# Kernel tuning notes

Measured on AMD Instinct MI355X. Metric: run time of the kernel, lower is better.

## Reference

```python
import jax, jax.numpy as jnp
import numpy as np

N = 50000
E = 800000
C = 128   # embed_channels
H = 4     # num_heads
D = C // H
POS = 3


def setup_inputs() -> dict:
    key = jax.random.key(0)
    ks = jax.random.split(key, 8)
    feat = jax.random.normal(ks[0], (N, C), dtype=jnp.float32)
    coord = jax.random.normal(ks[1], (N, POS), dtype=jnp.float32)
    graph = jax.random.randint(ks[2], (2, E), 0, N, dtype=jnp.int32)
    qkv_w = jax.random.normal(ks[3], (3 * C, C), dtype=jnp.float32) * (1.0 / np.sqrt(C))
    qkv_b = jax.random.normal(ks[4], (3 * C,), dtype=jnp.float32) * 0.02
    rpe_w = jax.random.normal(ks[5], (C, POS), dtype=jnp.float32) * (1.0 / np.sqrt(POS))
    rpe_b = jax.random.normal(ks[6], (C,), dtype=jnp.float32) * 0.02
    return {"feat": feat, "coord": coord, "graph": graph,
            "qkv_w": qkv_w, "qkv_b": qkv_b, "rpe_w": rpe_w, "rpe_b": rpe_b}


def _segment_softmax(x, seg, n):
    # x: [E, H], seg: [E] -> softmax over edges sharing the same destination node
    seg_max = jax.ops.segment_max(x, seg, num_segments=n)          # [N, H]
    seg_max = jnp.where(jnp.isfinite(seg_max), seg_max, 0.0)
    ex = jnp.exp(x - seg_max[seg])                                 # [E, H]
    seg_sum = jax.ops.segment_sum(ex, seg, num_segments=n)         # [N, H]
    return ex / seg_sum[seg]


def reference(feat, coord, graph, qkv_w, qkv_b, rpe_w, rpe_b):
    n = feat.shape[0]
    # qkv projection: [N, 3C] -> [N, 3, H, D]
    qkv = (feat @ qkv_w.T + qkv_b).reshape(n, 3, H, D)
    query, key, value = qkv[:, 0], qkv[:, 1], qkv[:, 2]            # each [N, H, D]
    dst, src = graph[0], graph[1]                                  # [E]
    # relative position encoding per edge
    rel = coord[dst] - coord[src]                                  # [E, 3]
    rpe = (rel @ rpe_w.T + rpe_b).reshape(-1, H, D)                # [E, H, D]
    # per-edge attention logits
    attn = (key[src] * query[dst] + rpe).sum(-1)                   # [E, H]
    attn = _segment_softmax(attn, dst, n)                          # [E, H]
    # weighted scatter-sum of values
    msg = attn[..., None] * value[src]                             # [E, H, D]
    out = jax.ops.segment_sum(msg, dst, num_segments=n)            # [N, H, D]
    return out.reshape(n, H * D)
```

## Files before the change

kernel.cpp:

```cpp
#include <hip/hip_runtime.h>
#include <hip/hip_bf16.h>

#define NN 50000
#define NE 800000
#define PAD 64
#define CAB 196
#define NBK 391
#define CAPB 2560
#define GB_STRIDE 32

typedef _Float16 fp16x8 __attribute__((ext_vector_type(8)));
typedef _Float16 half2 __attribute__((ext_vector_type(2)));
typedef __attribute__((ext_vector_type(8))) unsigned short ushort8;
typedef __attribute__((ext_vector_type(4))) float f32x4;

static __device__ __forceinline__ unsigned short f2h(float x) {
    _Float16 h = (_Float16)x;
    return __builtin_bit_cast(unsigned short, h);
}
static __device__ __forceinline__ float dot2(half2 a, half2 b, float c) {
#if __has_builtin(__builtin_amdgcn_fdot2)
    return __builtin_amdgcn_fdot2(a, b, c, false);
#else
    return c + (float)a.x * (float)b.x + (float)a.y * (float)b.y;
#endif
}
static __device__ __forceinline__ half2 h2(unsigned u) {
    return __builtin_bit_cast(half2, u);
}

__global__ __launch_bounds__(256) void qkv_gemm(
    const float* __restrict__ feat, const float* __restrict__ w,
    const float* __restrict__ bias, unsigned short* __restrict__ qbuf16,
    unsigned short* __restrict__ kvbuf,
    const float* __restrict__ coord, const float* __restrict__ rpe_w,
    const float* __restrict__ rpe_b, float* __restrict__ ca,
    float* __restrict__ cb,
    const int* __restrict__ graph, unsigned int* __restrict__ gbase,
    unsigned int* __restrict__ ebuf)
{
    const int t  = threadIdx.x;
    const int bx = blockIdx.x;
    int bi, role;
    if (bx < 1536) {
        int rem = bx & 31;
        role = rem >> 3;
        bi   = (bx >> 5) * 8 + (rem & 7);
    } else {
        int idx = bx - 1536;
        role = idx / 7;
        bi   = 384 + idx - role * 7;
    }

    __shared__ __align__(16) unsigned short Ah[128][40];
    __shared__ __align__(16) unsigned short Bh[128][40];

    if (role == 3) {
        unsigned int* hist  = (unsigned int*)&Ah[0][0];
        unsigned int* sbase = hist + 512;
        for (int u = t; u < NBK; u += 256) hist[u] = 0u;
        __syncthreads();

        int dsts[8], srcs[8];
        bool ok[8];
        const int e0 = bi * 2048;
#pragma unroll
        for (int u = 0; u < 8; ++u) {
            int e = e0 + u * 256 + t;
            ok[u] = (e < NE);
            if (ok[u]) { dsts[u] = graph[e]; srcs[u] = graph[NE + e]; }
        }
#pragma unroll
        for (int u = 0; u < 8; ++u)
            if (ok[u]) atomicAdd(&hist[dsts[u] >> 7], 1u);
        __syncthreads();
        for (int u = t; u < NBK; u += 256) {
            unsigned int c = hist[u];
            unsigned int s = c ? atomicAdd(&gbase[u * GB_STRIDE], c) : 0u;
            sbase[u] = s;
            hist[u]  = 0u;
        }
        __syncthreads();
#pragma unroll
        for (int u = 0; u < 8; ++u)
            if (ok[u]) {
                int b = dsts[u] >> 7;
                unsigned int pos = sbase[b] + atomicAdd(&hist[b], 1u);
                if (pos < CAPB)
                    ebuf[(size_t)b * CAPB + pos] =
                        ((unsigned int)(dsts[u] & 127) << 16) | (unsigned int)srcs[u];
            }

        if (bi < CAB) {
            __shared__ float s_rw[12];
            __shared__ float s_rb[4];
            if (t < 12) {
                int h = t / 3, p = t % 3;
                float s = 0.f;
                for (int d = 0; d < 32; ++d) s += rpe_w[(h * 32 + d) * 3 + p];
                s_rw[t] = s;
            } else if (t < 16) {
                int h = t - 12;
                float s = 0.f;
                for (int d = 0; d < 32; ++d) s += rpe_b[h * 32 + d];
                s_rb[h] = s;
            }
            __syncthreads();
            int n = bi * 256 + t;
            if (n < NN) {
                float c0 = coord[n * 3 + 0], c1 = coord[n * 3 + 1], c2 = coord[n * 3 + 2];
#pragma unroll
                for (int h = 0; h < 4; ++h) {
                    float a = c0 * s_rw[h * 3 + 0] + c1 * s_rw[h * 3 + 1] + c2 * s_rw[h * 3 + 2];
                    ca[n * 4 + h] = a;
                    cb[n * 4 + h] = a + s_rb[h];
                }
            }
        }
        return;
    }

    const int bm = bi * 128;
    const int bc = role * 128;

    const int wave = t >> 6;
    const int lane = t & 63;
    const int wr = wave & 1;
    const int wc = wave >> 1;
    const int qd = lane >> 4;
    const int l15 = lane & 15;

    f32x4 acc[4][4];
#pragma unroll
    for (int i = 0; i < 4; ++i)
#pragma unroll
        for (int j = 0; j < 4; ++j)
            acc[i][j] = (f32x4){0.f, 0.f, 0.f, 0.f};

    for (int ks = 0; ks < 4; ++ks) {
        const int k0 = ks * 32;
        if (ks) __syncthreads();
#pragma unroll
        for (int c = 0; c < 2; ++c) {
            int idx = c * 256 + t;
            int r  = idx >> 2;
            int c8 = (idx & 3) * 8;
            int ga = bm + r;
            ushort8 a8 = (ushort8){0,0,0,0,0,0,0,0};
            if (ga < NN) {
                const float* ap = feat + (size_t)ga * 128 + k0 + c8;
                float4 x = *(const float4*)ap;
                float4 y = *(const float4*)(ap + 4);
                a8 = (ushort8){f2h(x.x), f2h(x.y), f2h(x.z), f2h(x.w),
                               f2h(y.x), f2h(y.y), f2h(y.z), f2h(y.w)};
            }
            *(ushort8*)&Ah[r][c8] = a8;
            const float* bp = w + (size_t)(bc + r) * 128 + k0 + c8;
            float4 bx2 = *(const float4*)bp;
            float4 by2 = *(const float4*)(bp + 4);
            *(ushort8*)&Bh[r][c8] = (ushort8){f2h(bx2.x), f2h(bx2.y), f2h(bx2.z), f2h(bx2.w),
                                              f2h(by2.x), f2h(by2.y), f2h(by2.z), f2h(by2.w)};
        }
        __syncthreads();
        fp16x8 af[4];
#pragma unroll
        for (int i = 0; i < 4; ++i)
            af[i] = *(const fp16x8*)&Ah[wr * 64 + 16 * i + l15][qd * 8];
#pragma unroll
        for (int j = 0; j < 4; ++j) {
            fp16x8 bf = *(const fp16x8*)&Bh[wc * 64 + 16 * j + l15][qd * 8];
#pragma unroll
            for (int i = 0; i < 4; ++i)
                acc[i][j] = __builtin_amdgcn_mfma_f32_16x16x32_f16(af[i], bf, acc[i][j], 0, 0, 0);
        }
    }

    float bj[4];
#pragma unroll
    for (int j = 0; j < 4; ++j)
        bj[j] = bias[bc + wc * 64 + 16 * j + l15];

    unsigned short* Ct = &Ah[0][0];
    const int isQ = (role == 0);
    const int half = (role == 1) ? 0 : 128;
    const int relRowW = wr * 16 + qd * 4;

    for (int i = 0; i < 4; ++i) {
        __syncthreads();
#pragma unroll
        for (int j = 0; j < 4; ++j) {
            int col = wc * 64 + 16 * j + l15;
#pragma unroll
            for (int rg = 0; rg < 4; ++rg)
                Ct[(relRowW + rg) * 136 + col] = f2h(acc[i][j][rg] + bj[j]);
        }
        __syncthreads();
#pragma unroll
        for (int p = 0; p < 2; ++p) {
            int linear = p * 256 + t;
            int rr = linear >> 4;
            int cc = linear & 15;
            int absRow = bm + 16 * i + rr + ((rr >> 4) * 48);
            if (absRow < NN) {
                ushort8 val = *(const ushort8*)&Ct[rr * 136 + cc * 8];
                if (isQ) *(ushort8*)(qbuf16 + (size_t)absRow * 128 + cc * 8) = val;
                else     *(ushort8*)(kvbuf + (size_t)absRow * 256 + half + cc * 8) = val;
            }
        }
    }
}

__global__ __launch_bounds__(256) void attn_fused(
    const unsigned short* __restrict__ qbuf16, const unsigned short* __restrict__ kvbuf,
    const float* __restrict__ ca, const float* __restrict__ cb,
    const unsigned int* __restrict__ gbase, const unsigned int* __restrict__ ebuf,
    float* __restrict__ out)
{
    __shared__ __align__(16) unsigned short slots[32][64];
    __shared__ unsigned int ncnt[32];

    const int t    = threadIdx.x;
    const int b    = blockIdx.x >> 2;
    const int quad = blockIdx.x & 3;

    if (t < 32) ncnt[t] = 0u;
    __syncthreads();

    int total = (int)gbase[b * GB_STRIDE];
    if (total > CAPB) total = CAPB;
    const unsigned int* eb = ebuf + (size_t)b * CAPB;
    for (int i = t; i < total; i += 256) {
        unsigned int e = eb[i];
        int dl = (int)(e >> 16);
        if ((dl >> 5) == quad) {
            int ldl = dl & 31;
            unsigned int slot = atomicAdd(&ncnt[ldl], 1u);
            if (slot < PAD) slots[ldl][slot] = (unsigned short)(e & 0xFFFFu);
        }
    }
    __syncthreads();

    const int j  = t & 31;
    const int h  = j >> 3;
    const int j8 = j * 8;
    const int h4 = h * 4;
    const int ln = t >> 5;
    const char* kvp = (const char*)kvbuf;
    const char* cap = (const char*)ca;

    for (int g = 0; g < 4; ++g) {
        const int ldl = g * 8 + ln;
        const int n = b * 128 + quad * 32 + ldl;
        if (n >= NN) continue;
        int d = (int)ncnt[ldl];
        if (d > PAD) d = PAD;
        const unsigned short* sl = &slots[ldl][0];

        const uint2 qv = *(const uint2*)((const char*)qbuf16 + (size_t)n * 256 + j8);
        const half2 qh01 = h2(qv.x);
        const half2 qh23 = h2(qv.y);
        const float cbh = cb[n * 4 + h];

        float4 acc = make_float4(0.f, 0.f, 0.f, 0.f);
        float den = 0.f;

        int i = 0;
        for (; i + 7 < d; i += 8) {
            ushort8 s8 = *(const ushort8*)(sl + i);
            unsigned o[8];
#pragma unroll
            for (int u = 0; u < 8; ++u) o[u] = (unsigned)s8[u] << 9;
            uint2 kk[8], vv[8];
            float aa[8];
#pragma unroll
            for (int u = 0; u < 8; ++u) kk[u] = *(const uint2*)(kvp + o[u] + j8);
#pragma unroll
            for (int u = 0; u < 8; ++u) vv[u] = *(const uint2*)(kvp + o[u] + 256 + j8);
#pragma unroll
            for (int u = 0; u < 8; ++u) aa[u] = *(const float*)(cap + (o[u] >> 5) + h4);
            float p[8];
#pragma unroll
            for (int u = 0; u < 8; ++u)
                p[u] = dot2(qh01, h2(kk[u].x), dot2(qh23, h2(kk[u].y), 0.f));
#pragma unroll
            for (int u = 0; u < 8; ++u) p[u] += __shfl_xor(p[u], 1);
#pragma unroll
            for (int u = 0; u < 8; ++u) p[u] += __shfl_xor(p[u], 2);
#pragma unroll
            for (int u = 0; u < 8; ++u) p[u] += __shfl_xor(p[u], 4);
            float e[8];
#pragma unroll
            for (int u = 0; u < 8; ++u) { e[u] = __expf(p[u] + cbh - aa[u]); den += e[u]; }
#pragma unroll
            for (int u = 0; u < 8; ++u) {
                half2 va = h2(vv[u].x);
                half2 vb = h2(vv[u].y);
                acc.x += e[u] * (float)va.x;
                acc.y += e[u] * (float)va.y;
                acc.z += e[u] * (float)vb.x;
                acc.w += e[u] * (float)vb.y;
            }
        }
        for (; i + 3 < d; i += 4) {
            ushort4 s4 = *(const ushort4*)(sl + i);
            unsigned o0 = (unsigned)s4.x << 9;
            unsigned o1 = (unsigned)s4.y << 9;
            unsigned o2 = (unsigned)s4.z << 9;
            unsigned o3 = (unsigned)s4.w << 9;
            uint2 k0 = *(const uint2*)(kvp + o0 + j8);
            uint2 k1 = *(const uint2*)(kvp + o1 + j8);
            uint2 k2 = *(const uint2*)(kvp + o2 + j8);
            uint2 k3 = *(const uint2*)(kvp + o3 + j8);
            uint2 v0 = *(const uint2*)(kvp + o0 + 256 + j8);
            uint2 v1 = *(const uint2*)(kvp + o1 + 256 + j8);
            uint2 v2 = *(const uint2*)(kvp + o2 + 256 + j8);
            uint2 v3 = *(const uint2*)(kvp + o3 + 256 + j8);
            float a0 = *(const float*)(cap + (o0 >> 5) + h4);
            float a1 = *(const float*)(cap + (o1 >> 5) + h4);
            float a2 = *(const float*)(cap + (o2 >> 5) + h4);
            float a3 = *(const float*)(cap + (o3 >> 5) + h4);

            float p0 = dot2(qh01, h2(k0.x), dot2(qh23, h2(k0.y), 0.f));
            float p1 = dot2(qh01, h2(k1.x), dot2(qh23, h2(k1.y), 0.f));
            float p2 = dot2(qh01, h2(k2.x), dot2(qh23, h2(k2.y), 0.f));
            float p3 = dot2(qh01, h2(k3.x), dot2(qh23, h2(k3.y), 0.f));
            p0 += __shfl_xor(p0, 1); p1 += __shfl_xor(p1, 1);
            p2 += __shfl_xor(p2, 1); p3 += __shfl_xor(p3, 1);
            p0 += __shfl_xor(p0, 2); p1 += __shfl_xor(p1, 2);
            p2 += __shfl_xor(p2, 2); p3 += __shfl_xor(p3, 2);
            p0 += __shfl_xor(p0, 4); p1 += __shfl_xor(p1, 4);
            p2 += __shfl_xor(p2, 4); p3 += __shfl_xor(p3, 4);

            float e0 = __expf(p0 + cbh - a0);
            float e1 = __expf(p1 + cbh - a1);
            float e2 = __expf(p2 + cbh - a2);
            float e3 = __expf(p3 + cbh - a3);
            den += (e0 + e1) + (e2 + e3);
            half2 v0a = h2(v0.x), v0b = h2(v0.y);
            half2 v1a = h2(v1.x), v1b = h2(v1.y);
            half2 v2a = h2(v2.x), v2b = h2(v2.y);
            half2 v3a = h2(v3.x), v3b = h2(v3.y);
            acc.x += e0 * (float)v0a.x + e1 * (float)v1a.x + e2 * (float)v2a.x + e3 * (float)v3a.x;
            acc.y += e0 * (float)v0a.y + e1 * (float)v1a.y + e2 * (float)v2a.y + e3 * (float)v3a.y;
            acc.z += e0 * (float)v0b.x + e1 * (float)v1b.x + e2 * (float)v2b.x + e3 * (float)v3b.x;
            acc.w += e0 * (float)v0b.y + e1 * (float)v1b.y + e2 * (float)v2b.y + e3 * (float)v3b.y;
        }
        for (; i < d; ++i) {
            unsigned o0 = (unsigned)sl[i] << 9;
            uint2 k0 = *(const uint2*)(kvp + o0 + j8);
            uint2 v0 = *(const uint2*)(kvp + o0 + 256 + j8);
            float a0 = *(const float*)(cap + (o0 >> 5) + h4);
            float p0 = dot2(qh01, h2(k0.x), dot2(qh23, h2(k0.y), 0.f));
            p0 += __shfl_xor(p0, 1);
            p0 += __shfl_xor(p0, 2);
            p0 += __shfl_xor(p0, 4);
            float e = __expf(p0 + cbh - a0);
            den += e;
            half2 va = h2(v0.x);
            half2 vb = h2(v0.y);
            acc.x += e * (float)va.x;
            acc.y += e * (float)va.y;
            acc.z += e * (float)vb.x;
            acc.w += e * (float)vb.y;
        }

        float inv = (den > 0.f) ? 1.0f / den : 0.f;
        float4 o = make_float4(acc.x * inv, acc.y * inv, acc.z * inv, acc.w * inv);
        ((float4*)(out + (size_t)n * 128))[j] = o;
    }
}

extern "C" void kernel_launch(void* const* d_in, const int* in_sizes, int n_in,
                              void* d_out, int out_size, void* d_ws, size_t ws_size,
                              hipStream_t stream) {
    const float* feat  = (const float*)d_in[0];
    const float* coord = (const float*)d_in[1];
    const int*   graph = (const int*)d_in[2];
    const float* qkv_w = (const float*)d_in[3];
    const float* qkv_b = (const float*)d_in[4];
    const float* rpe_w = (const float*)d_in[5];
    const float* rpe_b = (const float*)d_in[6];
    float* out = (float*)d_out;

    unsigned short* qbuf16 = (unsigned short*)d_ws;
    unsigned short* kvbuf  = qbuf16 + (size_t)NN * 128;
    float* ca = (float*)(kvbuf + (size_t)NN * 256);
    float* cb = ca + (size_t)NN * 4;
    unsigned int* gbase = (unsigned int*)(cb + (size_t)NN * 4);
    unsigned int* ebuf  = gbase + (size_t)NBK * GB_STRIDE;

    hipMemsetAsync(gbase, 0, (size_t)NBK * GB_STRIDE * sizeof(unsigned int), stream);

    qkv_gemm  <<<dim3(391 * 4), 256, 0, stream>>>(feat, qkv_w, qkv_b, qbuf16, kvbuf,
                                                  coord, rpe_w, rpe_b, ca, cb,
                                                  graph, gbase, ebuf);
    attn_fused<<<dim3(NBK * 4), 256, 0, stream>>>(qbuf16, kvbuf, ca, cb,
                                                  gbase, ebuf, out);
}
```

Measured before the change: 182.1 us.

## Interleave K/V per lane and use ticket-based persistent attention blocks

The projection now writes K and V interleaved in 8-byte chunks, so each lane fetches its key and value slice with a single 16-byte gather per edge instead of two 8-byte gathers. The attention kernel becomes a persistent grid of 2048 blocks that grab work units (16 destination nodes each) from a global atomic ticket, replacing the static 4-way split of 32-node groups. This targets gather transaction count and load imbalance, at the cost of rescanning each bucket's edge list 8 times instead of 4, plus the atomic ticket traffic.

After: 214.9 us. 18.0% more time.

```diff
diff --git a/kernel.cpp b/kernel.cpp
--- a/kernel.cpp
+++ b/kernel.cpp
@@ -8,10 +8,13 @@
 #define NBK 391
 #define CAPB 2560
 #define GB_STRIDE 32
+#define NU 1564
+#define NOCT 3128
 
 typedef _Float16 fp16x8 __attribute__((ext_vector_type(8)));
 typedef _Float16 half2 __attribute__((ext_vector_type(2)));
 typedef __attribute__((ext_vector_type(8))) unsigned short ushort8;
+typedef __attribute__((ext_vector_type(4))) unsigned short u16x4;
 typedef __attribute__((ext_vector_type(4))) float f32x4;
 
 static __device__ __forceinline__ unsigned short f2h(float x) {
@@ -182,7 +185,7 @@
 
     unsigned short* Ct = &Ah[0][0];
     const int isQ = (role == 0);
-    const int half = (role == 1) ? 0 : 128;
+    const int vsel = (role == 2) ? 4 : 0;
     const int relRowW = wr * 16 + qd * 4;
 
     for (int i = 0; i < 4; ++i) {
@@ -203,8 +206,15 @@
             int absRow = bm + 16 * i + rr + ((rr >> 4) * 48);
             if (absRow < NN) {
                 ushort8 val = *(const ushort8*)&Ct[rr * 136 + cc * 8];
-                if (isQ) *(ushort8*)(qbuf16 + (size_t)absRow * 128 + cc * 8) = val;
-                else     *(ushort8*)(kvbuf + (size_t)absRow * 256 + half + cc * 8) = val;
+                if (isQ) {
+                    *(ushort8*)(qbuf16 + (size_t)absRow * 128 + cc * 8) = val;
+                } else {
+                    u16x4 lo = (u16x4){val[0], val[1], val[2], val[3]};
+                    u16x4 hi = (u16x4){val[4], val[5], val[6], val[7]};
+                    unsigned short* rowp = kvbuf + (size_t)absRow * 256;
+                    *(u16x4*)(rowp + cc * 16 + vsel)     = lo;
+                    *(u16x4*)(rowp + cc * 16 + 8 + vsel) = hi;
+                }
             }
         }
     }
@@ -214,159 +224,162 @@
     const unsigned short* __restrict__ qbuf16, const unsigned short* __restrict__ kvbuf,
     const float* __restrict__ ca, const float* __restrict__ cb,
     const unsigned int* __restrict__ gbase, const unsigned int* __restrict__ ebuf,
-    float* __restrict__ out)
+    unsigned int* __restrict__ ticket, float* __restrict__ out)
 {
-    __shared__ __align__(16) unsigned short slots[32][64];
-    __shared__ unsigned int ncnt[32];
-
-    const int t    = threadIdx.x;
-    const int b    = blockIdx.x >> 2;
-    const int quad = blockIdx.x & 3;
-
-    if (t < 32) ncnt[t] = 0u;
-    __syncthreads();
-
-    int total = (int)gbase[b * GB_STRIDE];
-    if (total > CAPB) total = CAPB;
-    const unsigned int* eb = ebuf + (size_t)b * CAPB;
-    for (int i = t; i < total; i += 256) {
-        unsigned int e = eb[i];
-        int dl = (int)(e >> 16);
-        if ((dl >> 5) == quad) {
-            int ldl = dl & 31;
-            unsigned int slot = atomicAdd(&ncnt[ldl], 1u);
-            if (slot < PAD) slots[ldl][slot] = (unsigned short)(e & 0xFFFFu);
-        }
-    }
-    __syncthreads();
-
-    const int j  = t & 31;
-    const int h  = j >> 3;
-    const int j8 = j * 8;
-    const int h4 = h * 4;
-    const int ln = t >> 5;
+    __shared__ __align__(16) unsigned short slots[16][64];
+    __shared__ unsigned int ncnt[16];
+    __shared__ unsigned int s_u;
+
+    const int t   = threadIdx.x;
+    const int j   = t & 31;
+    const int h   = j >> 3;
+    const int j16 = j * 16;
+    const int j8  = j * 8;
+    const int h4  = h * 4;
+    const int ln  = t >> 5;
     const char* kvp = (const char*)kvbuf;
     const char* cap = (const char*)ca;
 
-    for (int g = 0; g < 4; ++g) {
-        const int ldl = g * 8 + ln;
-        const int n = b * 128 + quad * 32 + ldl;
-        if (n >= NN) continue;
-        int d = (int)ncnt[ldl];
-        if (d > PAD) d = PAD;
-        const unsigned short* sl = &slots[ldl][0];
-
-        const uint2 qv = *(const uint2*)((const char*)qbuf16 + (size_t)n * 256 + j8);
-        const half2 qh01 = h2(qv.x);
-        const half2 qh23 = h2(qv.y);
-        const float cbh = cb[n * 4 + h];
-
-        float4 acc = make_float4(0.f, 0.f, 0.f, 0.f);
-        float den = 0.f;
-
-        int i = 0;
-        for (; i + 7 < d; i += 8) {
-            ushort8 s8 = *(const ushort8*)(sl + i);
-            unsigned o[8];
-#pragma unroll
-            for (int u = 0; u < 8; ++u) o[u] = (unsigned)s8[u] << 9;
-            uint2 kk[8], vv[8];
-            float aa[8];
-#pragma unroll
-            for (int u = 0; u < 8; ++u) kk[u] = *(const uint2*)(kvp + o[u] + j8);
-#pragma unroll
-            for (int u = 0; u < 8; ++u) vv[u] = *(const uint2*)(kvp + o[u] + 256 + j8);
-#pragma unroll
-            for (int u = 0; u < 8; ++u) aa[u] = *(const float*)(cap + (o[u] >> 5) + h4);
-            float p[8];
-#pragma unroll
-            for (int u = 0; u < 8; ++u)
-                p[u] = dot2(qh01, h2(kk[u].x), dot2(qh23, h2(kk[u].y), 0.f));
-#pragma unroll
-            for (int u = 0; u < 8; ++u) p[u] += __shfl_xor(p[u], 1);
-#pragma unroll
-            for (int u = 0; u < 8; ++u) p[u] += __shfl_xor(p[u], 2);
-#pragma unroll
-            for (int u = 0; u < 8; ++u) p[u] += __shfl_xor(p[u], 4);
-            float e[8];
-#pragma unroll
-            for (int u = 0; u < 8; ++u) { e[u] = __expf(p[u] + cbh - aa[u]); den += e[u]; }
-#pragma unroll
-            for (int u = 0; u < 8; ++u) {
-                half2 va = h2(vv[u].x);
-                half2 vb = h2(vv[u].y);
-                acc.x += e[u] * (float)va.x;
-                acc.y += e[u] * (float)va.y;
-                acc.z += e[u] * (float)vb.x;
-                acc.w += e[u] * (float)vb.y;
-            }
-        }
-        for (; i + 3 < d; i += 4) {
-            ushort4 s4 = *(const ushort4*)(sl + i);
-            unsigned o0 = (unsigned)s4.x << 9;
-            unsigned o1 = (unsigned)s4.y << 9;
-            unsigned o2 = (unsigned)s4.z << 9;
-            unsigned o3 = (unsigned)s4.w << 9;
-            uint2 k0 = *(const uint2*)(kvp + o0 + j8);
-            uint2 k1 = *(const uint2*)(kvp + o1 + j8);
-            uint2 k2 = *(const uint2*)(kvp + o2 + j8);
-            uint2 k3 = *(const uint2*)(kvp + o3 + j8);
-            uint2 v0 = *(const uint2*)(kvp + o0 + 256 + j8);
-            uint2 v1 = *(const uint2*)(kvp + o1 + 256 + j8);
-            uint2 v2 = *(const uint2*)(kvp + o2 + 256 + j8);
-            uint2 v3 = *(const uint2*)(kvp + o3 + 256 + j8);
-            float a0 = *(const float*)(cap + (o0 >> 5) + h4);
-            float a1 = *(const float*)(cap + (o1 >> 5) + h4);
-            float a2 = *(const float*)(cap + (o2 >> 5) + h4);
-            float a3 = *(const float*)(cap + (o3 >> 5) + h4);
-
-            float p0 = dot2(qh01, h2(k0.x), dot2(qh23, h2(k0.y), 0.f));
-            float p1 = dot2(qh01, h2(k1.x), dot2(qh23, h2(k1.y), 0.f));
-            float p2 = dot2(qh01, h2(k2.x), dot2(qh23, h2(k2.y), 0.f));
-            float p3 = dot2(qh01, h2(k3.x), dot2(qh23, h2(k3.y), 0.f));
-            p0 += __shfl_xor(p0, 1); p1 += __shfl_xor(p1, 1);
-            p2 += __shfl_xor(p2, 1); p3 += __shfl_xor(p3, 1);
-            p0 += __shfl_xor(p0, 2); p1 += __shfl_xor(p1, 2);
-            p2 += __shfl_xor(p2, 2); p3 += __shfl_xor(p3, 2);
-            p0 += __shfl_xor(p0, 4); p1 += __shfl_xor(p1, 4);
-            p2 += __shfl_xor(p2, 4); p3 += __shfl_xor(p3, 4);
-
-            float e0 = __expf(p0 + cbh - a0);
-            float e1 = __expf(p1 + cbh - a1);
-            float e2 = __expf(p2 + cbh - a2);
-            float e3 = __expf(p3 + cbh - a3);
-            den += (e0 + e1) + (e2 + e3);
-            half2 v0a = h2(v0.x), v0b = h2(v0.y);
-            half2 v1a = h2(v1.x), v1b = h2(v1.y);
-            half2 v2a = h2(v2.x), v2b = h2(v2.y);
-            half2 v3a = h2(v3.x), v3b = h2(v3.y);
-            acc.x += e0 * (float)v0a.x + e1 * (float)v1a.x + e2 * (float)v2a.x + e3 * (float)v3a.x;
-            acc.y += e0 * (float)v0a.y + e1 * (float)v1a.y + e2 * (float)v2a.y + e3 * (float)v3a.y;
-            acc.z += e0 * (float)v0b.x + e1 * (float)v1b.x + e2 * (float)v2b.x + e3 * (float)v3b.x;
-            acc.w += e0 * (float)v0b.y + e1 * (float)v1b.y + e2 * (float)v2b.y + e3 * (float)v3b.y;
-        }
-        for (; i < d; ++i) {
-            unsigned o0 = (unsigned)sl[i] << 9;
-            uint2 k0 = *(const uint2*)(kvp + o0 + j8);
-            uint2 v0 = *(const uint2*)(kvp + o0 + 256 + j8);
-            float a0 = *(const float*)(cap + (o0 >> 5) + h4);
-            float p0 = dot2(qh01, h2(k0.x), dot2(qh23, h2(k0.y), 0.f));
-            p0 += __shfl_xor(p0, 1);
-            p0 += __shfl_xor(p0, 2);
-            p0 += __shfl_xor(p0, 4);
-            float e = __expf(p0 + cbh - a0);
-            den += e;
-            half2 va = h2(v0.x);
-            half2 vb = h2(v0.y);
-            acc.x += e * (float)va.x;
-            acc.y += e * (float)va.y;
-            acc.z += e * (float)vb.x;
-            acc.w += e * (float)vb.y;
-        }
-
-        float inv = (den > 0.f) ? 1.0f / den : 0.f;
-        float4 o = make_float4(acc.x * inv, acc.y * inv, acc.z * inv, acc.w * inv);
-        ((float4*)(out + (size_t)n * 128))[j] = o;
+    for (;;) {
+        if (t == 0) s_u = atomicAdd(ticket, 1u);
+        __syncthreads();
+        const unsigned u = s_u;
+        if (u >= NOCT) return;
+        const int b  = (int)(u >> 3);
+        const int oc = (int)(u & 7);
+
+        if (t < 16) ncnt[t] = 0u;
+        __syncthreads();
+
+        int total = (int)gbase[b * GB_STRIDE];
+        if (total > CAPB) total = CAPB;
+        const unsigned int* eb = ebuf + (size_t)b * CAPB;
+        for (int i = t; i < total; i += 256) {
+            unsigned int e = eb[i];
+            int dl = (int)(e >> 16);
+            if ((dl >> 4) == oc) {
+                int ldl = dl & 15;
+                unsigned int slot = atomicAdd(&ncnt[ldl], 1u);
+                if (slot < PAD) slots[ldl][slot] = (unsigned short)(e & 0xFFFFu);
+            }
+        }
+        __syncthreads();
+
+        for (int g = 0; g < 2; ++g) {
+            const int ldl = g * 8 + ln;
+            const int n = b * 128 + oc * 16 + ldl;
+            if (n < NN) {
+                int d = (int)ncnt[ldl];
+                if (d > PAD) d = PAD;
+                const unsigned short* sl = &slots[ldl][0];
+
+                const uint2 qv = *(const uint2*)((const char*)qbuf16 + (size_t)n * 256 + j8);
+                const half2 qh01 = h2(qv.x);
+                const half2 qh23 = h2(qv.y);
+                const float cbh = cb[n * 4 + h];
+
+                float4 acc = make_float4(0.f, 0.f, 0.f, 0.f);
+                float den = 0.f;
+
+                int i = 0;
+                for (; i + 7 < d; i += 8) {
+                    ushort8 s8 = *(const ushort8*)(sl + i);
+                    unsigned o[8];
+#pragma unroll
+                    for (int v = 0; v < 8; ++v) o[v] = (unsigned)s8[v] << 9;
+                    uint4 kv[8];
+                    float aa[8];
+#pragma unroll
+                    for (int v = 0; v < 8; ++v) kv[v] = *(const uint4*)(kvp + o[v] + j16);
+#pragma unroll
+                    for (int v = 0; v < 8; ++v) aa[v] = *(const float*)(cap + (o[v] >> 5) + h4);
+                    float p[8];
+#pragma unroll
+                    for (int v = 0; v < 8; ++v)
+                        p[v] = dot2(qh01, h2(kv[v].x), dot2(qh23, h2(kv[v].y), 0.f));
+#pragma unroll
+                    for (int v = 0; v < 8; ++v) p[v] += __shfl_xor(p[v], 1);
+#pragma unroll
+                    for (int v = 0; v < 8; ++v) p[v] += __shfl_xor(p[v], 2);
+#pragma unroll
+                    for (int v = 0; v < 8; ++v) p[v] += __shfl_xor(p[v], 4);
+                    float e[8];
+#pragma unroll
+                    for (int v = 0; v < 8; ++v) { e[v] = __expf(p[v] + cbh - aa[v]); den += e[v]; }
+#pragma unroll
+                    for (int v = 0; v < 8; ++v) {
+                        half2 va = h2(kv[v].z);
+                        half2 vb = h2(kv[v].w);
+                        acc.x += e[v] * (float)va.x;
+                        acc.y += e[v] * (float)va.y;
+                        acc.z += e[v] * (float)vb.x;
+                        acc.w += e[v] * (float)vb.y;
+                    }
+                }
+                for (; i + 3 < d; i += 4) {
+                    ushort4 s4 = *(const ushort4*)(sl + i);
+                    unsigned o0 = (unsigned)s4.x << 9;
+                    unsigned o1 = (unsigned)s4.y << 9;
+                    unsigned o2 = (unsigned)s4.z << 9;
+                    unsigned o3 = (unsigned)s4.w << 9;
+                    uint4 k0 = *(const uint4*)(kvp + o0 + j16);
+                    uint4 k1 = *(const uint4*)(kvp + o1 + j16);
+                    uint4 k2 = *(const uint4*)(kvp + o2 + j16);
+                    uint4 k3 = *(const uint4*)(kvp + o3 + j16);
+                    float a0 = *(const float*)(cap + (o0 >> 5) + h4);
+                    float a1 = *(const float*)(cap + (o1 >> 5) + h4);
+                    float a2 = *(const float*)(cap + (o2 >> 5) + h4);
+                    float a3 = *(const float*)(cap + (o3 >> 5) + h4);
+
+                    float p0 = dot2(qh01, h2(k0.x), dot2(qh23, h2(k0.y), 0.f));
+                    float p1 = dot2(qh01, h2(k1.x), dot2(qh23, h2(k1.y), 0.f));
+                    float p2 = dot2(qh01, h2(k2.x), dot2(qh23, h2(k2.y), 0.f));
+                    float p3 = dot2(qh01, h2(k3.x), dot2(qh23, h2(k3.y), 0.f));
+                    p0 += __shfl_xor(p0, 1); p1 += __shfl_xor(p1, 1);
+                    p2 += __shfl_xor(p2, 1); p3 += __shfl_xor(p3, 1);
+                    p0 += __shfl_xor(p0, 2); p1 += __shfl_xor(p1, 2);
+                    p2 += __shfl_xor(p2, 2); p3 += __shfl_xor(p3, 2);
+                    p0 += __shfl_xor(p0, 4); p1 += __shfl_xor(p1, 4);
+                    p2 += __shfl_xor(p2, 4); p3 += __shfl_xor(p3, 4);
+
+                    float e0 = __expf(p0 + cbh - a0);
+                    float e1 = __expf(p1 + cbh - a1);
+                    float e2 = __expf(p2 + cbh - a2);
+                    float e3 = __expf(p3 + cbh - a3);
+                    den += (e0 + e1) + (e2 + e3);
+                    half2 v0a = h2(k0.z), v0b = h2(k0.w);
+                    half2 v1a = h2(k1.z), v1b = h2(k1.w);
+                    half2 v2a = h2(k2.z), v2b = h2(k2.w);
+                    half2 v3a = h2(k3.z), v3b = h2(k3.w);
+                    acc.x += e0 * (float)v0a.x + e1 * (float)v1a.x + e2 * (float)v2a.x + e3 * (float)v3a.x;
+                    acc.y += e0 * (float)v0a.y + e1 * (float)v1a.y + e2 * (float)v2a.y + e3 * (float)v3a.y;
+                    acc.z += e0 * (float)v0b.x + e1 * (float)v1b.x + e2 * (float)v2b.x + e3 * (float)v3b.x;
+                    acc.w += e0 * (float)v0b.y + e1 * (float)v1b.y + e2 * (float)v2b.y + e3 * (float)v3b.y;
+                }
+                for (; i < d; ++i) {
+                    unsigned o0 = (unsigned)sl[i] << 9;
+                    uint4 k0 = *(const uint4*)(kvp + o0 + j16);
+                    float a0 = *(const float*)(cap + (o0 >> 5) + h4);
+                    float p0 = dot2(qh01, h2(k0.x), dot2(qh23, h2(k0.y), 0.f));
+                    p0 += __shfl_xor(p0, 1);
+                    p0 += __shfl_xor(p0, 2);
+                    p0 += __shfl_xor(p0, 4);
+                    float e = __expf(p0 + cbh - a0);
+                    den += e;
+                    half2 va = h2(k0.z);
+                    half2 vb = h2(k0.w);
+                    acc.x += e * (float)va.x;
+                    acc.y += e * (float)va.y;
+                    acc.z += e * (float)vb.x;
+                    acc.w += e * (float)vb.y;
+                }
+
+                float inv = (den > 0.f) ? 1.0f / den : 0.f;
+                float4 o = make_float4(acc.x * inv, acc.y * inv, acc.z * inv, acc.w * inv);
+                ((float4*)(out + (size_t)n * 128))[j] = o;
+            }
+        }
+        __syncthreads();
     }
 }
 
@@ -386,14 +399,15 @@
     unsigned short* kvbuf  = qbuf16 + (size_t)NN * 128;
     float* ca = (float*)(kvbuf + (size_t)NN * 256);
     float* cb = ca + (size_t)NN * 4;
-    unsigned int* gbase = (unsigned int*)(cb + (size_t)NN * 4);
-    unsigned int* ebuf  = gbase + (size_t)NBK * GB_STRIDE;
-
-    hipMemsetAsync(gbase, 0, (size_t)NBK * GB_STRIDE * sizeof(unsigned int), stream);
-
-    qkv_gemm  <<<dim3(391 * 4), 256, 0, stream>>>(feat, qkv_w, qkv_b, qbuf16, kvbuf,
-                                                  coord, rpe_w, rpe_b, ca, cb,
-                                                  graph, gbase, ebuf);
-    attn_fused<<<dim3(NBK * 4), 256, 0, stream>>>(qbuf16, kvbuf, ca, cb,
-                                                  gbase, ebuf, out);
-}
+    unsigned int* gbase  = (unsigned int*)(cb + (size_t)NN * 4);
+    unsigned int* ticket = gbase + (size_t)NBK * GB_STRIDE;
+    unsigned int* ebuf   = ticket + GB_STRIDE;
+
+    hipMemsetAsync(gbase, 0, (size_t)(NBK + 1) * GB_STRIDE * sizeof(unsigned int), stream);
+
+    qkv_gemm  <<<dim3(NU), 256, 0, stream>>>(feat, qkv_w, qkv_b, qbuf16, kvbuf,
+                                             coord, rpe_w, rpe_b, ca, cb,
+                                             graph, gbase, ebuf);
+    attn_fused<<<dim3(2048), 256, 0, stream>>>(qbuf16, kvbuf, ca, cb,
+                                               gbase, ebuf, ticket, out);
+}
```

## Use persistent ticket-scheduled attention blocks over half-buckets of 64 nodes

Applied to the files above, without the earlier changes.

The attention kernel becomes persistent. A fixed grid of 2048 blocks pulls work units from a global atomic ticket, and each unit is half of a 128-node bucket (64 nodes) instead of a quarter. Each block now scans the bucket's edge list once per 64 nodes rather than once per 32, which halves the redundant edge-list scanning. Dynamic scheduling is also meant to balance uneven per-node degrees. In exchange, each unit carries a global atomic and an extra barrier, there are fewer units to spread across CUs, and the slot arrays in shared memory double in size.

Result: slower. 200.2 us (+9.9%).

```diff
diff --git a/kernel.cpp b/kernel.cpp
--- a/kernel.cpp
+++ b/kernel.cpp
@@ -8,6 +8,8 @@
 #define NBK 391
 #define CAPB 2560
 #define GB_STRIDE 32
+#define NU 1564
+#define NHALF 782
 
 typedef _Float16 fp16x8 __attribute__((ext_vector_type(8)));
 typedef _Float16 half2 __attribute__((ext_vector_type(2)));
@@ -214,32 +216,13 @@
     const unsigned short* __restrict__ qbuf16, const unsigned short* __restrict__ kvbuf,
     const float* __restrict__ ca, const float* __restrict__ cb,
     const unsigned int* __restrict__ gbase, const unsigned int* __restrict__ ebuf,
-    float* __restrict__ out)
+    unsigned int* __restrict__ ticket, float* __restrict__ out)
 {
-    __shared__ __align__(16) unsigned short slots[32][64];
-    __shared__ unsigned int ncnt[32];
-
-    const int t    = threadIdx.x;
-    const int b    = blockIdx.x >> 2;
-    const int quad = blockIdx.x & 3;
-
-    if (t < 32) ncnt[t] = 0u;
-    __syncthreads();
-
-    int total = (int)gbase[b * GB_STRIDE];
-    if (total > CAPB) total = CAPB;
-    const unsigned int* eb = ebuf + (size_t)b * CAPB;
-    for (int i = t; i < total; i += 256) {
-        unsigned int e = eb[i];
-        int dl = (int)(e >> 16);
-        if ((dl >> 5) == quad) {
-            int ldl = dl & 31;
-            unsigned int slot = atomicAdd(&ncnt[ldl], 1u);
-            if (slot < PAD) slots[ldl][slot] = (unsigned short)(e & 0xFFFFu);
-        }
-    }
-    __syncthreads();
-
+    __shared__ __align__(16) unsigned short slots[64][64];
+    __shared__ unsigned int ncnt[64];
+    __shared__ unsigned int s_u;
+
+    const int t  = threadIdx.x;
     const int j  = t & 31;
     const int h  = j >> 3;
     const int j8 = j * 8;
@@ -248,125 +231,153 @@
     const char* kvp = (const char*)kvbuf;
     const char* cap = (const char*)ca;
 
-    for (int g = 0; g < 4; ++g) {
-        const int ldl = g * 8 + ln;
-        const int n = b * 128 + quad * 32 + ldl;
-        if (n >= NN) continue;
-        int d = (int)ncnt[ldl];
-        if (d > PAD) d = PAD;
-        const unsigned short* sl = &slots[ldl][0];
-
-        const uint2 qv = *(const uint2*)((const char*)qbuf16 + (size_t)n * 256 + j8);
-        const half2 qh01 = h2(qv.x);
-        const half2 qh23 = h2(qv.y);
-        const float cbh = cb[n * 4 + h];
-
-        float4 acc = make_float4(0.f, 0.f, 0.f, 0.f);
-        float den = 0.f;
-
-        int i = 0;
-        for (; i + 7 < d; i += 8) {
-            ushort8 s8 = *(const ushort8*)(sl + i);
-            unsigned o[8];
-#pragma unroll
-            for (int u = 0; u < 8; ++u) o[u] = (unsigned)s8[u] << 9;
-            uint2 kk[8], vv[8];
-            float aa[8];
-#pragma unroll
-            for (int u = 0; u < 8; ++u) kk[u] = *(const uint2*)(kvp + o[u] + j8);
-#pragma unroll
-            for (int u = 0; u < 8; ++u) vv[u] = *(const uint2*)(kvp + o[u] + 256 + j8);
-#pragma unroll
-            for (int u = 0; u < 8; ++u) aa[u] = *(const float*)(cap + (o[u] >> 5) + h4);
-            float p[8];
-#pragma unroll
-            for (int u = 0; u < 8; ++u)
-                p[u] = dot2(qh01, h2(kk[u].x), dot2(qh23, h2(kk[u].y), 0.f));
-#pragma unroll
-            for (int u = 0; u < 8; ++u) p[u] += __shfl_xor(p[u], 1);
-#pragma unroll
-            for (int u = 0; u < 8; ++u) p[u] += __shfl_xor(p[u], 2);
-#pragma unroll
-            for (int u = 0; u < 8; ++u) p[u] += __shfl_xor(p[u], 4);
-            float e[8];
-#pragma unroll
-            for (int u = 0; u < 8; ++u) { e[u] = __expf(p[u] + cbh - aa[u]); den += e[u]; }
-#pragma unroll
-            for (int u = 0; u < 8; ++u) {
-                half2 va = h2(vv[u].x);
-                half2 vb = h2(vv[u].y);
-                acc.x += e[u] * (float)va.x;
-                acc.y += e[u] * (float)va.y;
-                acc.z += e[u] * (float)vb.x;
-                acc.w += e[u] * (float)vb.y;
-            }
-        }
-        for (; i + 3 < d; i += 4) {
-            ushort4 s4 = *(const ushort4*)(sl + i);
-            unsigned o0 = (unsigned)s4.x << 9;
-            unsigned o1 = (unsigned)s4.y << 9;
-            unsigned o2 = (unsigned)s4.z << 9;
-            unsigned o3 = (unsigned)s4.w << 9;
-            uint2 k0 = *(const uint2*)(kvp + o0 + j8);
-            uint2 k1 = *(const uint2*)(kvp + o1 + j8);
-            uint2 k2 = *(const uint2*)(kvp + o2 + j8);
-            uint2 k3 = *(const uint2*)(kvp + o3 + j8);
-            uint2 v0 = *(const uint2*)(kvp + o0 + 256 + j8);
-            uint2 v1 = *(const uint2*)(kvp + o1 + 256 + j8);
-            uint2 v2 = *(const uint2*)(kvp + o2 + 256 + j8);
-            uint2 v3 = *(const uint2*)(kvp + o3 + 256 + j8);
-            float a0 = *(const float*)(cap + (o0 >> 5) + h4);
-            float a1 = *(const float*)(cap + (o1 >> 5) + h4);
-            float a2 = *(const float*)(cap + (o2 >> 5) + h4);
-            float a3 = *(const float*)(cap + (o3 >> 5) + h4);
-
-            float p0 = dot2(qh01, h2(k0.x), dot2(qh23, h2(k0.y), 0.f));
-            float p1 = dot2(qh01, h2(k1.x), dot2(qh23, h2(k1.y), 0.f));
-            float p2 = dot2(qh01, h2(k2.x), dot2(qh23, h2(k2.y), 0.f));
-            float p3 = dot2(qh01, h2(k3.x), dot2(qh23, h2(k3.y), 0.f));
-            p0 += __shfl_xor(p0, 1); p1 += __shfl_xor(p1, 1);
-            p2 += __shfl_xor(p2, 1); p3 += __shfl_xor(p3, 1);
-            p0 += __shfl_xor(p0, 2); p1 += __shfl_xor(p1, 2);
-            p2 += __shfl_xor(p2, 2); p3 += __shfl_xor(p3, 2);
-            p0 += __shfl_xor(p0, 4); p1 += __shfl_xor(p1, 4);
-            p2 += __shfl_xor(p2, 4); p3 += __shfl_xor(p3, 4);
-
-            float e0 = __expf(p0 + cbh - a0);
-            float e1 = __expf(p1 + cbh - a1);
-            float e2 = __expf(p2 + cbh - a2);
-            float e3 = __expf(p3 + cbh - a3);
-            den += (e0 + e1) + (e2 + e3);
-            half2 v0a = h2(v0.x), v0b = h2(v0.y);
-            half2 v1a = h2(v1.x), v1b = h2(v1.y);
-            half2 v2a = h2(v2.x), v2b = h2(v2.y);
-            half2 v3a = h2(v3.x), v3b = h2(v3.y);
-            acc.x += e0 * (float)v0a.x + e1 * (float)v1a.x + e2 * (float)v2a.x + e3 * (float)v3a.x;
-            acc.y += e0 * (float)v0a.y + e1 * (float)v1a.y + e2 * (float)v2a.y + e3 * (float)v3a.y;
-            acc.z += e0 * (float)v0b.x + e1 * (float)v1b.x + e2 * (float)v2b.x + e3 * (float)v3b.x;
-            acc.w += e0 * (float)v0b.y + e1 * (float)v1b.y + e2 * (float)v2b.y + e3 * (float)v3b.y;
-        }
-        for (; i < d; ++i) {
-            unsigned o0 = (unsigned)sl[i] << 9;
-            uint2 k0 = *(const uint2*)(kvp + o0 + j8);
-            uint2 v0 = *(const uint2*)(kvp + o0 + 256 + j8);
-            float a0 = *(const float*)(cap + (o0 >> 5) + h4);
-            float p0 = dot2(qh01, h2(k0.x), dot2(qh23, h2(k0.y), 0.f));
-            p0 += __shfl_xor(p0, 1);
-            p0 += __shfl_xor(p0, 2);
-            p0 += __shfl_xor(p0, 4);
-            float e = __expf(p0 + cbh - a0);
-            den += e;
-            half2 va = h2(v0.x);
-            half2 vb = h2(v0.y);
-            acc.x += e * (float)va.x;
-            acc.y += e * (float)va.y;
-            acc.z += e * (float)vb.x;
-            acc.w += e * (float)vb.y;
-        }
-
-        float inv = (den > 0.f) ? 1.0f / den : 0.f;
-        float4 o = make_float4(acc.x * inv, acc.y * inv, acc.z * inv, acc.w * inv);
-        ((float4*)(out + (size_t)n * 128))[j] = o;
+    for (;;) {
+        if (t == 0) s_u = atomicAdd(ticket, 1u);
+        __syncthreads();
+        const unsigned u = s_u;
+        if (u >= NHALF) return;
+        const int b  = (int)(u >> 1);
+        const int hf = (int)(u & 1);
+
+        if (t < 64) ncnt[t] = 0u;
+        __syncthreads();
+
+        int total = (int)gbase[b * GB_STRIDE];
+        if (total > CAPB) total = CAPB;
+        const unsigned int* eb = ebuf + (size_t)b * CAPB;
+        for (int i = t; i < total; i += 256) {
+            unsigned int e = eb[i];
+            int dl = (int)(e >> 16);
+            if ((dl >> 6) == hf) {
+                int ldl = dl & 63;
+                unsigned int slot = atomicAdd(&ncnt[ldl], 1u);
+                if (slot < PAD) slots[ldl][slot] = (unsigned short)(e & 0xFFFFu);
+            }
+        }
+        __syncthreads();
+
+        for (int g = 0; g < 8; ++g) {
+            const int ldl = g * 8 + ln;
+            const int n = b * 128 + hf * 64 + ldl;
+            if (n < NN) {
+                int d = (int)ncnt[ldl];
+                if (d > PAD) d = PAD;
+                const unsigned short* sl = &slots[ldl][0];
+
+                const uint2 qv = *(const uint2*)((const char*)qbuf16 + (size_t)n * 256 + j8);
+                const half2 qh01 = h2(qv.x);
+                const half2 qh23 = h2(qv.y);
+                const float cbh = cb[n * 4 + h];
+
+                float4 acc = make_float4(0.f, 0.f, 0.f, 0.f);
+                float den = 0.f;
+
+                int i = 0;
+                for (; i + 7 < d; i += 8) {
+                    ushort8 s8 = *(const ushort8*)(sl + i);
+                    unsigned o[8];
+#pragma unroll
+                    for (int v = 0; v < 8; ++v) o[v] = (unsigned)s8[v] << 9;
+                    uint2 kk[8], vv[8];
+                    float aa[8];
+#pragma unroll
+                    for (int v = 0; v < 8; ++v) kk[v] = *(const uint2*)(kvp + o[v] + j8);
+#pragma unroll
+                    for (int v = 0; v < 8; ++v) vv[v] = *(const uint2*)(kvp + o[v] + 256 + j8);
+#pragma unroll
+                    for (int v = 0; v < 8; ++v) aa[v] = *(const float*)(cap + (o[v] >> 5) + h4);
+                    float p[8];
+#pragma unroll
+                    for (int v = 0; v < 8; ++v)
+                        p[v] = dot2(qh01, h2(kk[v].x), dot2(qh23, h2(kk[v].y), 0.f));
+#pragma unroll
+                    for (int v = 0; v < 8; ++v) p[v] += __shfl_xor(p[v], 1);
+#pragma unroll
+                    for (int v = 0; v < 8; ++v) p[v] += __shfl_xor(p[v], 2);
+#pragma unroll
+                    for (int v = 0; v < 8; ++v) p[v] += __shfl_xor(p[v], 4);
+                    float e[8];
+#pragma unroll
+                    for (int v = 0; v < 8; ++v) { e[v] = __expf(p[v] + cbh - aa[v]); den += e[v]; }
+#pragma unroll
+                    for (int v = 0; v < 8; ++v) {
+                        half2 va = h2(vv[v].x);
+                        half2 vb = h2(vv[v].y);
+                        acc.x += e[v] * (float)va.x;
+                        acc.y += e[v] * (float)va.y;
+                        acc.z += e[v] * (float)vb.x;
+                        acc.w += e[v] * (float)vb.y;
+                    }
+                }
+                for (; i + 3 < d; i += 4) {
+                    ushort4 s4 = *(const ushort4*)(sl + i);
+                    unsigned o0 = (unsigned)s4.x << 9;
+                    unsigned o1 = (unsigned)s4.y << 9;
+                    unsigned o2 = (unsigned)s4.z << 9;
+                    unsigned o3 = (unsigned)s4.w << 9;
+                    uint2 k0 = *(const uint2*)(kvp + o0 + j8);
+                    uint2 k1 = *(const uint2*)(kvp + o1 + j8);
+                    uint2 k2 = *(const uint2*)(kvp + o2 + j8);
+                    uint2 k3 = *(const uint2*)(kvp + o3 + j8);
+                    uint2 v0 = *(const uint2*)(kvp + o0 + 256 + j8);
+                    uint2 v1 = *(const uint2*)(kvp + o1 + 256 + j8);
+                    uint2 v2 = *(const uint2*)(kvp + o2 + 256 + j8);
+                    uint2 v3 = *(const uint2*)(kvp + o3 + 256 + j8);
+                    float a0 = *(const float*)(cap + (o0 >> 5) + h4);
+                    float a1 = *(const float*)(cap + (o1 >> 5) + h4);
+                    float a2 = *(const float*)(cap + (o2 >> 5) + h4);
+                    float a3 = *(const float*)(cap + (o3 >> 5) + h4);
+
+                    float p0 = dot2(qh01, h2(k0.x), dot2(qh23, h2(k0.y), 0.f));
+                    float p1 = dot2(qh01, h2(k1.x), dot2(qh23, h2(k1.y), 0.f));
+                    float p2 = dot2(qh01, h2(k2.x), dot2(qh23, h2(k2.y), 0.f));
+                    float p3 = dot2(qh01, h2(k3.x), dot2(qh23, h2(k3.y), 0.f));
+                    p0 += __shfl_xor(p0, 1); p1 += __shfl_xor(p1, 1);
+                    p2 += __shfl_xor(p2, 1); p3 += __shfl_xor(p3, 1);
+                    p0 += __shfl_xor(p0, 2); p1 += __shfl_xor(p1, 2);
+                    p2 += __shfl_xor(p2, 2); p3 += __shfl_xor(p3, 2);
+                    p0 += __shfl_xor(p0, 4); p1 += __shfl_xor(p1, 4);
+                    p2 += __shfl_xor(p2, 4); p3 += __shfl_xor(p3, 4);
+
+                    float e0 = __expf(p0 + cbh - a0);
+                    float e1 = __expf(p1 + cbh - a1);
+                    float e2 = __expf(p2 + cbh - a2);
+                    float e3 = __expf(p3 + cbh - a3);
+                    den += (e0 + e1) + (e2 + e3);
+                    half2 v0a = h2(v0.x), v0b = h2(v0.y);
+                    half2 v1a = h2(v1.x), v1b = h2(v1.y);
+                    half2 v2a = h2(v2.x), v2b = h2(v2.y);
+                    half2 v3a = h2(v3.x), v3b = h2(v3.y);
+                    acc.x += e0 * (float)v0a.x + e1 * (float)v1a.x + e2 * (float)v2a.x + e3 * (float)v3a.x;
+                    acc.y += e0 * (float)v0a.y + e1 * (float)v1a.y + e2 * (float)v2a.y + e3 * (float)v3a.y;
+                    acc.z += e0 * (float)v0b.x + e1 * (float)v1b.x + e2 * (float)v2b.x + e3 * (float)v3b.x;
+                    acc.w += e0 * (float)v0b.y + e1 * (float)v1b.y + e2 * (float)v2b.y + e3 * (float)v3b.y;
+                }
+                for (; i < d; ++i) {
+                    unsigned o0 = (unsigned)sl[i] << 9;
+                    uint2 k0 = *(const uint2*)(kvp + o0 + j8);
+                    uint2 v0 = *(const uint2*)(kvp + o0 + 256 + j8);
+                    float a0 = *(const float*)(cap + (o0 >> 5) + h4);
+                    float p0 = dot2(qh01, h2(k0.x), dot2(qh23, h2(k0.y), 0.f));
+                    p0 += __shfl_xor(p0, 1);
+                    p0 += __shfl_xor(p0, 2);
+                    p0 += __shfl_xor(p0, 4);
+                    float e = __expf(p0 + cbh - a0);
+                    den += e;
+                    half2 va = h2(v0.x);
+                    half2 vb = h2(v0.y);
+                    acc.x += e * (float)va.x;
+                    acc.y += e * (float)va.y;
+                    acc.z += e * (float)vb.x;
+                    acc.w += e * (float)vb.y;
+                }
+
+                float inv = (den > 0.f) ? 1.0f / den : 0.f;
+                float4 o = make_float4(acc.x * inv, acc.y * inv, acc.z * inv, acc.w * inv);
+                ((float4*)(out + (size_t)n * 128))[j] = o;
+            }
+        }
+        __syncthreads();
     }
 }
 
@@ -386,14 +397,15 @@
     unsigned short* kvbuf  = qbuf16 + (size_t)NN * 128;
     float* ca = (float*)(kvbuf + (size_t)NN * 256);
     float* cb = ca + (size_t)NN * 4;
-    unsigned int* gbase = (unsigned int*)(cb + (size_t)NN * 4);
-    unsigned int* ebuf  = gbase + (size_t)NBK * GB_STRIDE;
-
-    hipMemsetAsync(gbase, 0, (size_t)NBK * GB_STRIDE * sizeof(unsigned int), stream);
-
-    qkv_gemm  <<<dim3(391 * 4), 256, 0, stream>>>(feat, qkv_w, qkv_b, qbuf16, kvbuf,
-                                                  coord, rpe_w, rpe_b, ca, cb,
-                                                  graph, gbase, ebuf);
-    attn_fused<<<dim3(NBK * 4), 256, 0, stream>>>(qbuf16, kvbuf, ca, cb,
-                                                  gbase, ebuf, out);
-}
+    unsigned int* gbase  = (unsigned int*)(cb + (size_t)NN * 4);
+    unsigned int* ticket = gbase + (size_t)NBK * GB_STRIDE;
+    unsigned int* ebuf   = ticket + GB_STRIDE;
+
+    hipMemsetAsync(gbase, 0, (size_t)(NBK + 1) * GB_STRIDE * sizeof(unsigned int), stream);
+
+    qkv_gemm  <<<dim3(NU), 256, 0, stream>>>(feat, qkv_w, qkv_b, qbuf16, kvbuf,
+                                             coord, rpe_w, rpe_b, ca, cb,
+                                             graph, gbase, ebuf);
+    attn_fused<<<dim3(2048), 256, 0, stream>>>(qbuf16, kvbuf, ca, cb,
+                                               gbase, ebuf, ticket, out);
+}
```
